# Kernel optimization log

Measured on AMD Instinct MI355X. Metric: run time of the kernel, lower is better.

## Reference

```python
import jax, jax.numpy as jnp
import numpy as np

HID, HEADS, DH, L = 64, 8, 8, 2  # hidden_dim, num_heads, head_dim, num_layers


def setup_inputs() -> dict:
    key = jax.random.key(0)
    ks = jax.random.split(key, 18)
    B, S, N, Cin, Cout, E = 4, 12, 512, 3, 3, 8192
    p = lambda k, shape: (jax.random.normal(k, shape, jnp.float32) * 0.05)
    return {
        "x": jax.random.normal(ks[0], (B, S, N, Cin), jnp.float32),
        "edge_index": jax.random.randint(ks[1], (2, E), 0, N),
        "Win": p(ks[2], (HID, Cin)), "b_in": p(ks[3], (HID,)),
        "Wqs": p(ks[4], (L, HID, HID)), "bqs": p(ks[5], (L, HID)),
        "Wks": p(ks[6], (L, HID, HID)), "bks": p(ks[7], (L, HID)),
        "Wvs": p(ks[8], (L, HID, HID)), "bvs": p(ks[9], (L, HID)),
        "Wqt": p(ks[10], (L, HID, HID)), "bqt": p(ks[11], (L, HID)),
        "Wkt": p(ks[12], (L, HID, HID)), "bkt": p(ks[13], (L, HID)),
        "Wvt": p(ks[14], (L, HID, HID)), "bvt": p(ks[15], (L, HID)),
        "Wout": p(ks[16], (Cout, HID)), "bout": p(ks[17], (Cout,)),
    }


def reference(x, edge_index, Win, b_in, Wqs, bqs, Wks, bks, Wvs, bvs,
              Wqt, bqt, Wkt, bkt, Wvt, bvt, Wout, bout):
    B, S, N, _ = x.shape
    scale = 1.0 / np.sqrt(DH).astype(np.float32)
    # input projection: [B,S,N,Cin] -> [B,S,N,HID]
    h = x @ Win.T + b_in
    # dense NxN edge mask, exactly as the torch module builds it
    mask = jnp.zeros((N, N), jnp.float32).at[edge_index[0], edge_index[1]].set(1.0)
    for l in range(L):
        # ---- spatial attention (over nodes, per (batch, time)) ----
        q = (h @ Wqs[l].T + bqs[l]).reshape(B, S, N, HEADS, DH)
        k = (h @ Wks[l].T + bks[l]).reshape(B, S, N, HEADS, DH)
        v = (h @ Wvs[l].T + bvs[l]).reshape(B, S, N, HEADS, DH)
        s = jnp.einsum('bsnhd,bsmhd->bshnm', q, k) * scale  # [B,S,H,N,N]
        s = jnp.where(mask[None, None, None] == 0, jnp.float32(-1e9), s)
        a = jax.nn.softmax(s, axis=-1)
        h = jnp.einsum('bshnm,bsmhd->bsnhd', a, v).reshape(B, S, N, HID)
        # ---- temporal attention (over seq, per (batch, node)) ----
        q = (h @ Wqt[l].T + bqt[l]).reshape(B, S, N, HEADS, DH)
        k = (h @ Wkt[l].T + bkt[l]).reshape(B, S, N, HEADS, DH)
        v = (h @ Wvt[l].T + bvt[l]).reshape(B, S, N, HEADS, DH)
        s = jnp.einsum('bsnhd,btnhd->bnhst', q, k) * scale  # [B,N,H,S,S]
        a = jax.nn.softmax(s, axis=-1)
        h = jnp.einsum('bnhst,btnhd->bsnhd', a, v).reshape(B, S, N, HID)
    # take last time step, project to out_channels
    return h[:, -1] @ Wout.T + bout
```

## Files before the change

kernel.cpp:

```cpp
#include <hip/hip_runtime.h>
#include <hip/hip_bf16.h>

#define HIDN   64
#define NHEADS 8
#define DHEAD  8
#define NLAY   2
#define BB     4
#define SS     12
#define NNODE  512
#define NEDGE  8192
#define XELEMS (BB * SS * NNODE * 3)
#define ROWS   (BB * SS * NNODE)
#define QSCALE 0.51006967f

typedef unsigned short u16;
typedef unsigned int   u32;
typedef __attribute__((ext_vector_type(4))) float f4;
typedef __attribute__((ext_vector_type(8))) short s8v;

__device__ __forceinline__ float b2f(u16 u) {
    union { u32 i; float f; } c; c.i = ((u32)u) << 16; return c.f;
}
__device__ __forceinline__ u16 f2b(float f) {
    union { float f; u32 i; } c; c.f = f;
    u32 r = c.i + 0x7FFFu + ((c.i >> 16) & 1u);
    return (u16)(r >> 16);
}
__device__ __forceinline__ u32 pk2(float a, float b) {
    return (u32)f2b(a) | ((u32)f2b(b) << 16);
}
__device__ __forceinline__ float ld(const void* p, int i, int fl) {
    return fl ? ((const float*)p)[i] : b2f(((const u16*)p)[i]);
}

__global__ void detect_kernel(const u16* __restrict__ x, int* __restrict__ flag) {
    int i0 = blockIdx.x * 256 + threadIdx.x;
    int bad = 0;
    for (int i = i0; i < XELEMS; i += 64 * 256) {
        float v = fabsf(b2f(x[i]));
        if (!(v <= 100.f)) bad = 1;
    }
    if (bad) atomicOr(flag, 1);
}

struct PrepArgs {
    const void* x; const void* Win; const void* bin; u16* h;
    const void* Wq[2]; const void* bq[2];
    const void* Wk[2]; const void* bk[2];
    const void* Wv[2]; const void* bv[2];
    u16* wb; u16* whd; float* bp[2];
    const int* ei; int* row_ptr; u16* col_idx;
};
__global__ __launch_bounds__(512) void prep_kernel(PrepArgs a, const int* __restrict__ flagp) {
    __shared__ u32 msk[NNODE * 16];
    __shared__ int sc[512];
    int fl = (*flagp != 0);
    int bid = blockIdx.x;
    int tid = threadIdx.x;
    if (bid < 384) {
        int base = (bid * 512 + tid) * 8;
        int row = base >> 6, j0 = base & 63;
        float x0 = ld(a.x, row * 3, fl);
        float x1 = ld(a.x, row * 3 + 1, fl);
        float x2 = ld(a.x, row * 3 + 2, fl);
        float o[8];
#pragma unroll
        for (int jj = 0; jj < 8; ++jj) {
            int j = j0 + jj;
            o[jj] = ld(a.bin, j, fl) + x0 * ld(a.Win, j * 3, fl)
                  + x1 * ld(a.Win, j * 3 + 1, fl) + x2 * ld(a.Win, j * 3 + 2, fl);
        }
        *(uint4*)&a.h[base] = make_uint4(pk2(o[0], o[1]), pk2(o[2], o[3]),
                                         pk2(o[4], o[5]), pk2(o[6], o[7]));
        return;
    }
    if (bid < 432) {
        int u = (bid - 384) * 512 + tid;
        int l = u / 12288;
        int t = u - l * 12288;
        int j = t >> 6, i = t & 63;
        int cg = j >> 6, cc = j & 63;
        const void* W = (cg == 0) ? a.Wq[1] : (cg == 1) ? a.Wk[1] : a.Wv[1];
        a.wb[u] = f2b(ld(W, l * 4096 + cc * 64 + i, fl));
        if (u < 768) {
            int p2 = u / 384;
            int r3 = u - p2 * 384;
            int l2 = r3 / 192;
            int j2 = r3 - l2 * 192;
            int cg2 = j2 >> 6;
            const void* B = (cg2 == 0) ? a.bq[p2] : (cg2 == 1) ? a.bk[p2] : a.bv[p2];
            a.bp[p2][l2 * 192 + j2] = ld(B, l2 * 64 + (j2 & 63), fl);
        }
        return;
    }
    if (bid < 496) {
        int u = (bid - 432) * 512 + tid;
        int l    = u >> 14;
        int rem  = u & 16383;
        int hd   = rem >> 11;
        int rem2 = rem & 2047;
        int tile = rem2 >> 10;
        int rem3 = rem2 & 1023;
        int c    = rem3 >> 6;
        int i    = rem3 & 63;
        int j;
        if (tile == 0) j = (c < 8) ? (64 + hd * 8 + c) : (128 + hd * 8 + (c - 8));
        else           j = (c < 8) ? (hd * 8 + c) : -1;
        u16 val = 0;
        if (j >= 0) {
            int cg = j >> 6, cc = j & 63;
            const void* W = (cg == 0) ? a.Wq[0] : (cg == 1) ? a.Wk[0] : a.Wv[0];
            val = f2b(ld(W, l * 4096 + cc * 64 + i, fl));
        }
        a.whd[u] = val;
        return;
    }
    for (int i = tid; i < NNODE * 16; i += 512) msk[i] = 0;
    __syncthreads();
    for (int e = tid; e < NEDGE; e += 512) {
        int r = a.ei[e];
        int m = a.ei[NEDGE + e];
        atomicOr(&msk[r * 16 + (m >> 5)], 1u << (m & 31));
    }
    __syncthreads();
    int n = tid;
    u32 w[16];
    int d = 0;
#pragma unroll
    for (int i = 0; i < 16; ++i) { w[i] = msk[n * 16 + i]; d += __popc(w[i]); }
    sc[n] = d;
    __syncthreads();
    for (int s = 1; s < 512; s <<= 1) {
        int v = (n >= s) ? sc[n - s] : 0;
        __syncthreads();
        sc[n] += v;
        __syncthreads();
    }
    int excl = sc[n] - d;
    a.row_ptr[n] = excl;
    if (n == 511) a.row_ptr[512] = sc[511];
    int base = excl;
#pragma unroll
    for (int i = 0; i < 16; ++i) {
        u32 m = w[i];
        while (m) {
            int b = __ffs(m) - 1;
            m &= m - 1;
            a.col_idx[base++] = (u16)(i * 32 + b);
        }
    }
}

__global__ __launch_bounds__(256) void spat_fused_kernel(
    const u16* __restrict__ hb, const u16* __restrict__ whd,
    const float* __restrict__ bp,
    const int* __restrict__ row_ptr, const u16* __restrict__ col_idx,
    u16* __restrict__ h2) {
    __shared__ __align__(16) float Ks[NNODE][8];
    __shared__ __align__(16) float Vs[NNODE][8];
    __shared__ float qS[256][9];
    int bxx = blockIdx.x;
    int pair = bxx >> 1, half = bxx & 1;
    int bs = pair >> 3, hd = pair & 7;
    int t = threadIdx.x;
    int lane = t & 63, wv = t >> 6;
    int lrow = lane & 15, kg = lane >> 4;
    const u16* hsl = hb + (long)bs * NNODE * HIDN;
    const u16* wkv = whd + hd * 2048;
    const u16* wq  = whd + hd * 2048 + 1024;
    s8v bkv0 = *(const s8v*)(wkv + lrow * 64 + kg * 8);
    s8v bkv1 = *(const s8v*)(wkv + lrow * 64 + kg * 8 + 32);
    s8v bq0  = *(const s8v*)(wq  + lrow * 64 + kg * 8);
    s8v bq1  = *(const s8v*)(wq  + lrow * 64 + kg * 8 + 32);
    float biasKV = (lrow < 8) ? bp[64 + hd * 8 + lrow] : bp[128 + hd * 8 + (lrow & 7)];
    float biasQ  = bp[hd * 8 + (lrow & 7)];
#pragma unroll
    for (int s = 0; s < 8; ++s) {
        int rt = wv * 8 + s;
        const u16* ap = hsl + (rt * 16 + lrow) * 64 + kg * 8;
        s8v ha0 = *(const s8v*)ap;
        s8v ha1 = *(const s8v*)(ap + 32);
        f4 acc = (f4){0.f, 0.f, 0.f, 0.f};
        acc = __builtin_amdgcn_mfma_f32_16x16x32_bf16(ha0, bkv0, acc, 0, 0, 0);
        acc = __builtin_amdgcn_mfma_f32_16x16x32_bf16(ha1, bkv1, acc, 0, 0, 0);
        int node = rt * 16 + kg * 4;
        if (lrow < 8) {
#pragma unroll
            for (int r = 0; r < 4; ++r) Ks[node + r][lrow] = acc[r] + biasKV;
        } else {
#pragma unroll
            for (int r = 0; r < 4; ++r) Vs[node + r][lrow & 7] = acc[r] + biasKV;
        }
    }
#pragma unroll
    for (int s = 0; s < 4; ++s) {
        int rtq = wv * 4 + s;
        const u16* ap = hsl + (half * 256 + rtq * 16 + lrow) * 64 + kg * 8;
        s8v ha0 = *(const s8v*)ap;
        s8v ha1 = *(const s8v*)(ap + 32);
        f4 acc = (f4){0.f, 0.f, 0.f, 0.f};
        acc = __builtin_amdgcn_mfma_f32_16x16x32_bf16(ha0, bq0, acc, 0, 0, 0);
        acc = __builtin_amdgcn_mfma_f32_16x16x32_bf16(ha1, bq1, acc, 0, 0, 0);
        if (lrow < 8) {
            int nl = rtq * 16 + kg * 4;
#pragma unroll
            for (int r = 0; r < 4; ++r) qS[nl + r][lrow] = (acc[r] + biasQ) * QSCALE;
        }
    }
    __syncthreads();
    int n = half * 256 + t;
    float4 qa = make_float4(qS[t][0], qS[t][1], qS[t][2], qS[t][3]);
    float4 qc = make_float4(qS[t][4], qS[t][5], qS[t][6], qS[t][7]);
    int e0 = row_ptr[n], e1 = row_ptr[n + 1];
    float l = 0.f;
    float o0=0.f,o1=0.f,o2=0.f,o3=0.f,o4=0.f,o5=0.f,o6=0.f,o7=0.f;
    for (int e = e0; e < e1; ++e) {
        int m = col_idx[e];
        float4 ka = *(const float4*)&Ks[m][0];
        float4 kc = *(const float4*)&Ks[m][4];
        float s = qa.x*ka.x + qa.y*ka.y + qa.z*ka.z + qa.w*ka.w
                + qc.x*kc.x + qc.y*kc.y + qc.z*kc.z + qc.w*kc.w;
        float p = exp2f(s);
        l += p;
        float4 va = *(const float4*)&Vs[m][0];
        float4 vc = *(const float4*)&Vs[m][4];
        o0 += p*va.x; o1 += p*va.y; o2 += p*va.z; o3 += p*va.w;
        o4 += p*vc.x; o5 += p*vc.y; o6 += p*vc.z; o7 += p*vc.w;
    }
    if (e1 == e0) {
        for (int m = 0; m < NNODE; ++m) {
            o0 += Vs[m][0]; o1 += Vs[m][1]; o2 += Vs[m][2]; o3 += Vs[m][3];
            o4 += Vs[m][4]; o5 += Vs[m][5]; o6 += Vs[m][6]; o7 += Vs[m][7];
        }
        l = (float)NNODE;
    }
    float inv = 1.f / l;
    u16* op = h2 + ((long)(bs * NNODE + n)) * HIDN + hd * 8;
    *(uint4*)op = make_uint4(pk2(o0*inv, o1*inv), pk2(o2*inv, o3*inv),
                             pk2(o4*inv, o5*inv), pk2(o6*inv, o7*inv));
}

__global__ __launch_bounds__(384) void temp_fused_kernel(
    const u16* __restrict__ h2b, const u16* __restrict__ wb,
    const float* __restrict__ bp, u16* __restrict__ h) {
    __shared__ float S[3][SS][32][9];
    int b  = blockIdx.x >> 7;
    int n0 = (blockIdx.x & 127) * 4;
    int t = threadIdx.x;
    int lane = t & 63, wv = t >> 6;
    int lrow = lane & 15, kg = lane >> 4;
    int rt  = wv >> 1;
    int ct0 = (wv & 1) * 6;
    int gr = rt * 16 + lrow;
    int tta = gr >> 2, nla = gr & 3;
    const u16* ap = h2b + ((long)((b * SS + tta) * NNODE) + n0 + nla) * HIDN + kg * 8;
    s8v haf0 = *(const s8v*)ap;
    s8v haf1 = *(const s8v*)(ap + 32);
#pragma unroll
    for (int s = 0; s < 6; ++s) {
        int ct = ct0 + s;
        const u16* wp = wb + (ct * 16 + lrow) * 64 + kg * 8;
        s8v wb0 = *(const s8v*)wp;
        s8v wb1 = *(const s8v*)(wp + 32);
        f4 acc = (f4){0.f, 0.f, 0.f, 0.f};
        acc = __builtin_amdgcn_mfma_f32_16x16x32_bf16(haf0, wb0, acc, 0, 0, 0);
        acc = __builtin_amdgcn_mfma_f32_16x16x32_bf16(haf1, wb1, acc, 0, 0, 0);
        int j = ct * 16 + lrow;
        float bb = bp[j];
        int tz = j >> 6, cc = j & 63, hd2 = cc >> 3, dh = cc & 7;
#pragma unroll
        for (int r = 0; r < 4; ++r) {
            int gr2 = rt * 16 + kg * 4 + r;
            S[tz][gr2 >> 2][(gr2 & 3) * 8 + hd2][dh] = acc[r] + bb;
        }
    }
    __syncthreads();
    int sq = t >> 5, r = t & 31;
    int nl = r >> 3, hd = r & 7;
    const float* qd = &S[0][sq][r][0];
    float q0=qd[0],q1=qd[1],q2=qd[2],q3=qd[3],q4=qd[4],q5=qd[5],q6=qd[6],q7=qd[7];
    float s[SS];
#pragma unroll
    for (int tt = 0; tt < SS; ++tt) {
        const float* kd = &S[1][tt][r][0];
        s[tt] = (q0 * kd[0] + q1 * kd[1] + q2 * kd[2] + q3 * kd[3] +
                 q4 * kd[4] + q5 * kd[5] + q6 * kd[6] + q7 * kd[7]) * QSCALE;
    }
    float mx = s[0];
#pragma unroll
    for (int tt = 1; tt < SS; ++tt) mx = fmaxf(mx, s[tt]);
    float l = 0.f;
#pragma unroll
    for (int tt = 0; tt < SS; ++tt) { s[tt] = exp2f(s[tt] - mx); l += s[tt]; }
    float a0=0.f,a1=0.f,a2=0.f,a3=0.f,a4=0.f,a5=0.f,a6=0.f,a7=0.f;
#pragma unroll
    for (int tt = 0; tt < SS; ++tt) {
        const float* vd = &S[2][tt][r][0];
        float e = s[tt];
        a0 += e * vd[0]; a1 += e * vd[1]; a2 += e * vd[2]; a3 += e * vd[3];
        a4 += e * vd[4]; a5 += e * vd[5]; a6 += e * vd[6]; a7 += e * vd[7];
    }
    float inv = 1.f / l;
    u16* op = h + ((long)((b * SS + sq) * NNODE) + n0 + nl) * HIDN + hd * 8;
    *(uint4*)op = make_uint4(pk2(a0*inv, a1*inv), pk2(a2*inv, a3*inv),
                             pk2(a4*inv, a5*inv), pk2(a6*inv, a7*inv));
}

__global__ void out_proj_kernel(const u16* __restrict__ h, const void* __restrict__ W,
                                const void* __restrict__ b, void* __restrict__ out,
                                const int* __restrict__ flagp) {
    int fl = (*flagp != 0);
    int t = blockIdx.x * blockDim.x + threadIdx.x;
    if (t >= BB * NNODE * 3) return;
    int c  = t % 3;
    int bn = t / 3;
    int n  = bn & (NNODE - 1);
    int bb = bn >> 9;
    const u16* hp = h + ((long)((bb * SS + (SS - 1)) * NNODE + n)) * HIDN;
    float a = ld(b, c, fl);
#pragma unroll
    for (int i = 0; i < HIDN; i += 8) {
        uint4 hv = *(const uint4*)&hp[i];
        const u32 hw[4] = {hv.x, hv.y, hv.z, hv.w};
#pragma unroll
        for (int j2 = 0; j2 < 4; ++j2) {
            float hlo = b2f((u16)(hw[j2] & 0xFFFF));
            float hhi = b2f((u16)(hw[j2] >> 16));
            a += hlo * ld(W, c * 64 + i + j2 * 2,     fl)
               + hhi * ld(W, c * 64 + i + j2 * 2 + 1, fl);
        }
    }
    if (fl) ((float*)out)[t] = a;
    else    ((__hip_bfloat16*)out)[t] = __float2bfloat16(a);
}

extern "C" void kernel_launch(void* const* d_in, const int* in_sizes, int n_in,
                              void* d_out, int out_size, void* d_ws, size_t ws_size,
                              hipStream_t stream) {
    const int* ei = (const int*)d_in[1];

    float* ws = (float*)d_ws;
    int*   flag    = (int*)ws;
    int*   row_ptr = (int*)(ws + 64);
    u16*   col_idx = (u16*)(ws + 640);
    u16*   wb16  = (u16*)(ws + 4736);
    u16*   whd16 = (u16*)(ws + 4736 + 12288);
    float* bsp   = ws + 4736 + 12288 + 16384;
    float* btp   = bsp + 384;
    u16*   hb16  = (u16*)(btp + 384);
    u16*   h2b16 = hb16 + ROWS * HIDN;

    int flv = -1;
    if (in_sizes) {
        if (in_sizes[0] == XELEMS * 2) flv = 0;
        else if (in_sizes[0] == XELEMS * 4) flv = 1;
    }
    if (flv >= 0) {
        (void)hipMemsetAsync(flag, flv, sizeof(int), stream);
    } else {
        (void)hipMemsetAsync(flag, 0, sizeof(int), stream);
        detect_kernel<<<64, 256, 0, stream>>>((const u16*)d_in[0], flag);
    }

    PrepArgs pr;
    pr.x = d_in[0]; pr.Win = d_in[2]; pr.bin = d_in[3]; pr.h = hb16;
    pr.Wq[0] = d_in[4];  pr.bq[0] = d_in[5];
    pr.Wk[0] = d_in[6];  pr.bk[0] = d_in[7];
    pr.Wv[0] = d_in[8];  pr.bv[0] = d_in[9];
    pr.Wq[1] = d_in[10]; pr.bq[1] = d_in[11];
    pr.Wk[1] = d_in[12]; pr.bk[1] = d_in[13];
    pr.Wv[1] = d_in[14]; pr.bv[1] = d_in[15];
    pr.wb = wb16; pr.whd = whd16; pr.bp[0] = bsp; pr.bp[1] = btp;
    pr.ei = ei; pr.row_ptr = row_ptr; pr.col_idx = col_idx;
    prep_kernel<<<384 + 48 + 64 + 1, 512, 0, stream>>>(pr, flag);

    for (int l = 0; l < NLAY; ++l) {
        spat_fused_kernel<<<BB * SS * NHEADS * 2, 256, 0, stream>>>(
            hb16, whd16 + l * 16384, bsp + l * 192, row_ptr, col_idx, h2b16);
        temp_fused_kernel<<<BB * (NNODE / 4), 384, 0, stream>>>(
            h2b16, wb16 + l * 12288, btp + l * 192, hb16);
    }
    out_proj_kernel<<<(BB * NNODE * 3 + 255) / 256, 256, 0, stream>>>(
        hb16, d_in[16], d_in[17], d_out, flag);
}
```

Baseline: 183.1 us.

## Merge spatial block halves and fuse output projection into last temporal kernel

The spatial attention kernel now runs one 512-thread block per (batch,time,head) instead of two 256-thread halves. Previously each half recomputed the full K/V projection for all 512 nodes, so this removes that duplicated work. The output projection is folded into the final temporal kernel, which stages last-timestep rows in shared memory and computes the 3 outputs there, dropping one kernel launch. In exchange there are half as many spatial blocks, which lowers parallelism, plus a larger shared footprint and a block-wide barrier in the temporal kernel.

```diff
diff --git a/kernel.cpp b/kernel.cpp
--- a/kernel.cpp
+++ b/kernel.cpp
@@ -151,16 +151,15 @@
     }
 }
 
-__global__ __launch_bounds__(256) void spat_fused_kernel(
+__global__ __launch_bounds__(512) void spat_fused_kernel(
     const u16* __restrict__ hb, const u16* __restrict__ whd,
     const float* __restrict__ bp,
     const int* __restrict__ row_ptr, const u16* __restrict__ col_idx,
     u16* __restrict__ h2) {
     __shared__ __align__(16) float Ks[NNODE][8];
     __shared__ __align__(16) float Vs[NNODE][8];
-    __shared__ float qS[256][9];
-    int bxx = blockIdx.x;
-    int pair = bxx >> 1, half = bxx & 1;
+    __shared__ float qS[NNODE][9];
+    int pair = blockIdx.x;
     int bs = pair >> 3, hd = pair & 7;
     int t = threadIdx.x;
     int lane = t & 63, wv = t >> 6;
@@ -175,8 +174,8 @@
     float biasKV = (lrow < 8) ? bp[64 + hd * 8 + lrow] : bp[128 + hd * 8 + (lrow & 7)];
     float biasQ  = bp[hd * 8 + (lrow & 7)];
 #pragma unroll
-    for (int s = 0; s < 8; ++s) {
-        int rt = wv * 8 + s;
+    for (int s = 0; s < 4; ++s) {
+        int rt = wv * 4 + s;
         const u16* ap = hsl + (rt * 16 + lrow) * 64 + kg * 8;
         s8v ha0 = *(const s8v*)ap;
         s8v ha1 = *(const s8v*)(ap + 32);
@@ -194,23 +193,23 @@
     }
 #pragma unroll
     for (int s = 0; s < 4; ++s) {
-        int rtq = wv * 4 + s;
-        const u16* ap = hsl + (half * 256 + rtq * 16 + lrow) * 64 + kg * 8;
+        int rt = wv * 4 + s;
+        const u16* ap = hsl + (rt * 16 + lrow) * 64 + kg * 8;
         s8v ha0 = *(const s8v*)ap;
         s8v ha1 = *(const s8v*)(ap + 32);
         f4 acc = (f4){0.f, 0.f, 0.f, 0.f};
         acc = __builtin_amdgcn_mfma_f32_16x16x32_bf16(ha0, bq0, acc, 0, 0, 0);
         acc = __builtin_amdgcn_mfma_f32_16x16x32_bf16(ha1, bq1, acc, 0, 0, 0);
         if (lrow < 8) {
-            int nl = rtq * 16 + kg * 4;
+            int nl = rt * 16 + kg * 4;
 #pragma unroll
             for (int r = 0; r < 4; ++r) qS[nl + r][lrow] = (acc[r] + biasQ) * QSCALE;
         }
     }
     __syncthreads();
-    int n = half * 256 + t;
-    float4 qa = make_float4(qS[t][0], qS[t][1], qS[t][2], qS[t][3]);
-    float4 qc = make_float4(qS[t][4], qS[t][5], qS[t][6], qS[t][7]);
+    int n = t;
+    float4 qa = make_float4(qS[n][0], qS[n][1], qS[n][2], qS[n][3]);
+    float4 qc = make_float4(qS[n][4], qS[n][5], qS[n][6], qS[n][7]);
     int e0 = row_ptr[n], e1 = row_ptr[n + 1];
     float l = 0.f;
     float o0=0.f,o1=0.f,o2=0.f,o3=0.f,o4=0.f,o5=0.f,o6=0.f,o7=0.f;
@@ -242,8 +241,11 @@
 
 __global__ __launch_bounds__(384) void temp_fused_kernel(
     const u16* __restrict__ h2b, const u16* __restrict__ wb,
-    const float* __restrict__ bp, u16* __restrict__ h) {
+    const float* __restrict__ bp, u16* __restrict__ h,
+    const void* __restrict__ Wout, const void* __restrict__ bout,
+    void* __restrict__ out, const int* __restrict__ flagp, int last) {
     __shared__ float S[3][SS][32][9];
+    __shared__ u32 outS[4][32];
     int b  = blockIdx.x >> 7;
     int n0 = (blockIdx.x & 127) * 4;
     int t = threadIdx.x;
@@ -301,37 +303,42 @@
         a4 += e * vd[4]; a5 += e * vd[5]; a6 += e * vd[6]; a7 += e * vd[7];
     }
     float inv = 1.f / l;
+    u32 p0 = pk2(a0*inv, a1*inv), p1 = pk2(a2*inv, a3*inv);
+    u32 p2 = pk2(a4*inv, a5*inv), p3 = pk2(a6*inv, a7*inv);
     u16* op = h + ((long)((b * SS + sq) * NNODE) + n0 + nl) * HIDN + hd * 8;
-    *(uint4*)op = make_uint4(pk2(a0*inv, a1*inv), pk2(a2*inv, a3*inv),
-                             pk2(a4*inv, a5*inv), pk2(a6*inv, a7*inv));
-}
-
-__global__ void out_proj_kernel(const u16* __restrict__ h, const void* __restrict__ W,
-                                const void* __restrict__ b, void* __restrict__ out,
-                                const int* __restrict__ flagp) {
-    int fl = (*flagp != 0);
-    int t = blockIdx.x * blockDim.x + threadIdx.x;
-    if (t >= BB * NNODE * 3) return;
-    int c  = t % 3;
-    int bn = t / 3;
-    int n  = bn & (NNODE - 1);
-    int bb = bn >> 9;
-    const u16* hp = h + ((long)((bb * SS + (SS - 1)) * NNODE + n)) * HIDN;
-    float a = ld(b, c, fl);
-#pragma unroll
-    for (int i = 0; i < HIDN; i += 8) {
-        uint4 hv = *(const uint4*)&hp[i];
-        const u32 hw[4] = {hv.x, hv.y, hv.z, hv.w};
-#pragma unroll
-        for (int j2 = 0; j2 < 4; ++j2) {
-            float hlo = b2f((u16)(hw[j2] & 0xFFFF));
-            float hhi = b2f((u16)(hw[j2] >> 16));
-            a += hlo * ld(W, c * 64 + i + j2 * 2,     fl)
-               + hhi * ld(W, c * 64 + i + j2 * 2 + 1, fl);
-        }
-    }
-    if (fl) ((float*)out)[t] = a;
-    else    ((__hip_bfloat16*)out)[t] = __float2bfloat16(a);
+    *(uint4*)op = make_uint4(p0, p1, p2, p3);
+    if (last) {
+        if (sq == SS - 1) {
+            outS[nl][hd * 4 + 0] = p0;
+            outS[nl][hd * 4 + 1] = p1;
+            outS[nl][hd * 4 + 2] = p2;
+            outS[nl][hd * 4 + 3] = p3;
+        }
+        __syncthreads();
+        if (t < 12) {
+            int fl = (*flagp != 0);
+            int c = t % 3, nl2 = t / 3;
+            float acc = ld(bout, c, fl);
+#pragma unroll
+            for (int i = 0; i < HIDN; i += 8) {
+                u32 hw0 = outS[nl2][i / 2 + 0];
+                u32 hw1 = outS[nl2][i / 2 + 1];
+                u32 hw2 = outS[nl2][i / 2 + 2];
+                u32 hw3 = outS[nl2][i / 2 + 3];
+                const u32 hw[4] = {hw0, hw1, hw2, hw3};
+#pragma unroll
+                for (int j2 = 0; j2 < 4; ++j2) {
+                    float hlo = b2f((u16)(hw[j2] & 0xFFFF));
+                    float hhi = b2f((u16)(hw[j2] >> 16));
+                    acc += hlo * ld(Wout, c * 64 + i + j2 * 2,     fl)
+                         + hhi * ld(Wout, c * 64 + i + j2 * 2 + 1, fl);
+                }
+            }
+            int ti = (b * NNODE + n0 + nl2) * 3 + c;
+            if (fl) ((float*)out)[ti] = acc;
+            else    ((__hip_bfloat16*)out)[ti] = __float2bfloat16(acc);
+        }
+    }
 }
 
 extern "C" void kernel_launch(void* const* d_in, const int* in_sizes, int n_in,
@@ -375,11 +382,10 @@
     prep_kernel<<<384 + 48 + 64 + 1, 512, 0, stream>>>(pr, flag);
 
     for (int l = 0; l < NLAY; ++l) {
-        spat_fused_kernel<<<BB * SS * NHEADS * 2, 256, 0, stream>>>(
+        spat_fused_kernel<<<BB * SS * NHEADS, 512, 0, stream>>>(
             hb16, whd16 + l * 16384, bsp + l * 192, row_ptr, col_idx, h2b16);
         temp_fused_kernel<<<BB * (NNODE / 4), 384, 0, stream>>>(
-            h2b16, wb16 + l * 12288, btp + l * 192, hb16);
-    }
-    out_proj_kernel<<<(BB * NNODE * 3 + 255) / 256, 256, 0, stream>>>(
-        hb16, d_in[16], d_in[17], d_out, flag);
-}
+            h2b16, wb16 + l * 12288, btp + l * 192, hb16,
+            d_in[16], d_in[17], d_out, flag, (l == NLAY - 1) ? 1 : 0);
+    }
+}
```

After: 171.6 us. 1.07x faster.
